# Performance work log

Measured on AMD Instinct MI355X. Metric: run time of the kernel, lower is better.

The kernel has to match this reference:

```python
import jax, jax.numpy as jnp
import numpy as np

B, NPG, C = 16, 4096, 256          # graphs, nodes per graph per type, feat dim
N = B * NPG                        # nodes per type
E = N * 16                         # edges per edge type (avg degree 16)
RATIO = 0.25
K = int(np.ceil(RATIO * NPG))      # top-k nodes per graph per type


def setup_inputs() -> dict:
    key = jax.random.key(0)
    ks = jax.random.split(key, 16)
    s = 1.0 / np.sqrt(C)
    inp = {
        "x_inst": jax.random.normal(ks[0], (N, C), jnp.float32),
        "x_data": jax.random.normal(ks[1], (N, C), jnp.float32),
        "w_kqv_inst": jax.random.normal(ks[2], (C, 3), jnp.float32) * s,
        "b_kqv_inst": jnp.zeros((3,), jnp.float32),
        "w_kqv_data": jax.random.normal(ks[3], (C, 3), jnp.float32) * s,
        "b_kqv_data": jnp.zeros((3,), jnp.float32),
        "w_out_inst": jax.random.normal(ks[4], (1, 1), jnp.float32),
        "b_out_inst": jnp.zeros((1,), jnp.float32),
        "w_out_data": jax.random.normal(ks[5], (1, 1), jnp.float32),
        "b_out_data": jnp.zeros((1,), jnp.float32),
        "krel_w": jax.random.normal(ks[6], (3,), jnp.float32),
        "krel_b": jnp.zeros((3,), jnp.float32),
        "vrel_w": jax.random.normal(ks[7], (3,), jnp.float32),
        "vrel_b": jnp.zeros((3,), jnp.float32),
        "p_rel": jnp.ones((3,), jnp.float32),
        "ei_i2d": jax.random.randint(ks[8], (2, E), 0, N, jnp.int32),
        "ei_d2i": jax.random.randint(ks[9], (2, E), 0, N, jnp.int32),
        "ei_i2i": jax.random.randint(ks[10], (2, E), 0, N, jnp.int32),
        "batch_inst": jnp.repeat(jnp.arange(B, dtype=jnp.int32), NPG),
        "batch_data": jnp.repeat(jnp.arange(B, dtype=jnp.int32), NPG),
    }
    return inp


def _hgt_scores(x_inst, x_data, w_kqv_inst, b_kqv_inst, w_kqv_data, b_kqv_data,
                w_out_inst, b_out_inst, w_out_data, b_out_data,
                krel_w, krel_b, vrel_w, vrel_b, p_rel,
                ei_i2d, ei_d2i, ei_i2i):
    # HGTConv with out_channels=1, heads=1 -> H=1, D=1 (k,q,v scalar per node)
    kqv_i = x_inst @ w_kqv_inst + b_kqv_inst   # [N,3]
    kqv_d = x_data @ w_kqv_data + b_kqv_data
    k_i, q_i, v_i = kqv_i[:, 0], kqv_i[:, 1], kqv_i[:, 2]
    k_d, q_d, v_d = kqv_d[:, 0], kqv_d[:, 1], kqv_d[:, 2]
    # dst offsets follow node-type order: inst=0, data=N
    q_glob = jnp.concatenate([q_i, q_d])       # [2N]
    Ntot = 2 * N

    def edge_terms(k_src, v_src, ei, t, dst_off):
        s, d = ei[0], ei[1]
        ke = k_src[s] * krel_w[t] + krel_b[t]  # per-relation 1x1 k_rel
        ve = v_src[s] * vrel_w[t] + vrel_b[t]  # per-relation 1x1 v_rel
        dg = d + dst_off
        logit = q_glob[dg] * ke * p_rel[t]     # (q_i*k_j).sum * p_rel / sqrt(D=1)
        return logit, ve, dg

    l0, v0, d0 = edge_terms(k_i, v_i, ei_i2d, 0, N)  # inst->data (dst=data)
    l1, v1, d1 = edge_terms(k_d, v_d, ei_d2i, 1, 0)  # data->inst (dst=inst)
    l2, v2, d2 = edge_terms(k_i, v_i, ei_i2i, 2, 0)  # inst->inst (dst=inst)
    logits = jnp.concatenate([l0, l1, l2])
    vals = jnp.concatenate([v0, v1, v2])
    dst = jnp.concatenate([d0, d1, d2])

    # segment softmax over incoming edges of each destination node
    m = jax.ops.segment_max(logits, dst, num_segments=Ntot)
    m = jnp.where(jnp.isfinite(m), m, 0.0)
    ex = jnp.exp(logits - m[dst])
    den = jax.ops.segment_sum(ex, dst, num_segments=Ntot)
    alpha = ex / den[dst]
    a = jax.ops.segment_sum(alpha * vals, dst, num_segments=Ntot)  # [2N]

    # out_lin (1->1) per node type; skip inactive (1 != 256); GELU (exact)
    s_i = jax.nn.gelu(a[:N, None] * w_out_inst[0, 0] + b_out_inst, approximate=False)
    s_d = jax.nn.gelu(a[N:, None] * w_out_data[0, 0] + b_out_data, approximate=False)
    return s_i, s_d  # [N,1] each


def _pool(x, score):
    # per-graph top-k on score, gate by tanh(score), mean over selected
    sv = score[:, 0].reshape(B, NPG)
    xv = x.reshape(B, NPG, -1)
    topv, topi = jax.lax.top_k(sv, K)                      # [B,K]
    xs = jnp.take_along_axis(xv, topi[:, :, None], axis=1)  # [B,K,C]
    return (xs * jnp.tanh(topv)[:, :, None]).mean(axis=1)   # [B,C]


def reference(x_inst, x_data, w_kqv_inst, b_kqv_inst, w_kqv_data, b_kqv_data,
              w_out_inst, b_out_inst, w_out_data, b_out_data,
              krel_w, krel_b, vrel_w, vrel_b, p_rel,
              ei_i2d, ei_d2i, ei_i2i, batch_inst, batch_data):
    # batch_* are uniform [B x NPG] blocks; pooling uses reshape equivalently.
    s_i, s_d = _hgt_scores(x_inst, x_data, w_kqv_inst, b_kqv_inst,
                           w_kqv_data, b_kqv_data, w_out_inst, b_out_inst,
                           w_out_data, b_out_data, krel_w, krel_b,
                           vrel_w, vrel_b, p_rel, ei_i2d, ei_d2i, ei_i2i)
    return jnp.concatenate([_pool(x_inst, s_i), _pool(x_data, s_d)], axis=-1)  # [B, 2C]
```

## Files before the change

### kernel.cpp

```cpp
#include <hip/hip_runtime.h>
#include <math.h>

constexpr int BB   = 16;
constexpr int NPGc = 4096;
constexpr int Cc   = 256;
constexpr int Nc   = BB * NPGc;
constexpr int Ec   = Nc * 16;
constexpr int Kc   = 1024;
constexpr int NBUK = 1024;
constexpr int BUKW = 128;
constexpr int CHUNK = 16384;
constexpr int NCHUNK = (3 * Ec) / CHUNK;

__device__ __forceinline__ unsigned long long dkey(double f) {
    long long b = __double_as_longlong(f);
    unsigned long long u = (unsigned long long)b;
    return (b < 0) ? ~u : (u | 0x8000000000000000ULL);
}
__device__ __forceinline__ double inv_dkey(unsigned long long u) {
    unsigned long long b = (u & 0x8000000000000000ULL) ? (u ^ 0x8000000000000000ULL) : ~u;
    return __longlong_as_double((long long)b);
}

__global__ __launch_bounds__(256) void kqv_kernel(
    const float* __restrict__ x_inst, const float* __restrict__ x_data,
    const float* __restrict__ w_inst, const float* __restrict__ b_inst,
    const float* __restrict__ w_data, const float* __restrict__ b_data,
    double* __restrict__ k_i, double* __restrict__ v_i,
    double* __restrict__ k_d, double* __restrict__ v_d,
    double* __restrict__ q_glob)
{
    int tid  = threadIdx.x;
    int wave = tid >> 6, lane = tid & 63;
    int grp  = lane >> 4, l = lane & 15;
    int row  = blockIdx.x * 16 + wave * 4 + grp;
    int side = (row >= Nc) ? 1 : 0;
    int node = row - side * Nc;
    const float* x  = side ? x_data : x_inst;
    const float* w  = side ? w_data : w_inst;
    const float* bb = side ? b_data : b_inst;

    const float4* rp = (const float4*)(x + (size_t)node * Cc);
    double kk = 0.0, qq = 0.0, vv = 0.0;
#pragma unroll
    for (int it = 0; it < 4; ++it) {
        float4 xv = rp[it * 16 + l];
        float xs[4] = {xv.x, xv.y, xv.z, xv.w};
        int cbase = it * 64 + l * 4;
#pragma unroll
        for (int u = 0; u < 4; ++u) {
            double xd = (double)xs[u];
            const float* wp = w + (cbase + u) * 3;
            kk += xd * (double)wp[0];
            qq += xd * (double)wp[1];
            vv += xd * (double)wp[2];
        }
    }
#pragma unroll
    for (int off = 8; off; off >>= 1) {
        kk += __shfl_xor(kk, off, 64);
        qq += __shfl_xor(qq, off, 64);
        vv += __shfl_xor(vv, off, 64);
    }
    if (l == 0) {
        kk += (double)bb[0]; qq += (double)bb[1]; vv += (double)bb[2];
        if (side) { k_d[node] = kk; v_d[node] = vv; q_glob[Nc + node] = qq; }
        else      { k_i[node] = kk; v_i[node] = vv; q_glob[node]      = qq; }
    }
}

__device__ __forceinline__ int edge_dg(const int* ei0, const int* ei1,
                                       const int* ei2, unsigned e) {
    int t = (int)(e >> 20);
    int i = (int)(e & (unsigned)(Ec - 1));
    const int* ei = (t == 0) ? ei0 : (t == 1) ? ei1 : ei2;
    int d = ei[Ec + i];
    return d + ((t == 0) ? Nc : 0);
}

__global__ __launch_bounds__(256) void count_kernel(
    const int* __restrict__ ei0, const int* __restrict__ ei1,
    const int* __restrict__ ei2, unsigned* __restrict__ bucket_cnt)
{
    __shared__ unsigned hist[NBUK];
    int tid = threadIdx.x;
    for (int j = tid; j < NBUK; j += 256) hist[j] = 0;
    __syncthreads();
    unsigned base = blockIdx.x * (unsigned)CHUNK;
#pragma unroll 4
    for (int j = 0; j < CHUNK / 256; ++j) {
        unsigned e = base + j * 256 + tid;
        int dg = edge_dg(ei0, ei1, ei2, e);
        atomicAdd(&hist[dg >> 7], 1u);
    }
    __syncthreads();
    for (int j = tid; j < NBUK; j += 256)
        if (hist[j]) atomicAdd(&bucket_cnt[j], hist[j]);
}

__global__ __launch_bounds__(1024) void scan_kernel(
    const unsigned* __restrict__ bucket_cnt,
    unsigned* __restrict__ bucket_base, unsigned* __restrict__ bucket_fill)
{
    __shared__ unsigned s[NBUK];
    int t = threadIdx.x;
    unsigned mine = bucket_cnt[t];
    s[t] = mine;
    __syncthreads();
    for (int off = 1; off < NBUK; off <<= 1) {
        unsigned v = (t >= off) ? s[t - off] : 0u;
        __syncthreads();
        s[t] += v;
        __syncthreads();
    }
    unsigned ex = s[t] - mine;
    bucket_base[t] = ex;
    bucket_fill[t] = ex;
    if (t == NBUK - 1) bucket_base[NBUK] = s[t];
}

__global__ __launch_bounds__(256) void fill_kernel(
    const int* __restrict__ ei0, const int* __restrict__ ei1,
    const int* __restrict__ ei2, unsigned* __restrict__ bucket_fill,
    unsigned* __restrict__ sorted)
{
    __shared__ unsigned hist[NBUK];
    __shared__ unsigned res[NBUK];
    int tid = threadIdx.x;
    for (int j = tid; j < NBUK; j += 256) hist[j] = 0;
    __syncthreads();
    unsigned base = blockIdx.x * (unsigned)CHUNK;
#pragma unroll 4
    for (int j = 0; j < CHUNK / 256; ++j) {
        unsigned e = base + j * 256 + tid;
        int dg = edge_dg(ei0, ei1, ei2, e);
        atomicAdd(&hist[dg >> 7], 1u);
    }
    __syncthreads();
    for (int j = tid; j < NBUK; j += 256) {
        unsigned h = hist[j];
        res[j] = h ? atomicAdd(&bucket_fill[j], h) : 0u;
        hist[j] = 0;
    }
    __syncthreads();
#pragma unroll 4
    for (int j = 0; j < CHUNK / 256; ++j) {
        unsigned e = base + j * 256 + tid;
        int t = (int)(e >> 20);
        int i = (int)(e & (unsigned)(Ec - 1));
        const int* ei = (t == 0) ? ei0 : (t == 1) ? ei1 : ei2;
        int dg = ei[Ec + i] + ((t == 0) ? Nc : 0);
        int bkt = dg >> 7;
        unsigned local = atomicAdd(&hist[bkt], 1u);
        sorted[res[bkt] + local] =
            (unsigned)i | ((unsigned)t << 20) | ((unsigned)(dg & 127) << 22);
    }
}

__global__ __launch_bounds__(256) void bucket_accum_kernel(
    const unsigned* __restrict__ bucket_base, const unsigned* __restrict__ sorted,
    const int* __restrict__ ei0, const int* __restrict__ ei1,
    const int* __restrict__ ei2,
    const float* __restrict__ krel_w, const float* __restrict__ krel_b,
    const float* __restrict__ vrel_w, const float* __restrict__ vrel_b,
    const float* __restrict__ p_rel,
    const double* __restrict__ k_i, const double* __restrict__ v_i,
    const double* __restrict__ k_d, const double* __restrict__ v_d,
    const double* __restrict__ q_glob,
    double* __restrict__ den, double* __restrict__ num)
{
    __shared__ double den_l[BUKW];
    __shared__ double num_l[BUKW];
    __shared__ double q_l[BUKW];
    int tid = threadIdx.x;
    int b   = blockIdx.x;
    if (tid < BUKW) {
        den_l[tid] = 0.0;
        num_l[tid] = 0.0;
        q_l[tid]   = q_glob[b * BUKW + tid];
    }
    double kw0 = krel_w[0], kw1 = krel_w[1], kw2 = krel_w[2];
    double kb0 = krel_b[0], kb1 = krel_b[1], kb2 = krel_b[2];
    double vw0 = vrel_w[0], vw1 = vrel_w[1], vw2 = vrel_w[2];
    double vb0 = vrel_b[0], vb1 = vrel_b[1], vb2 = vrel_b[2];
    double pr0 = p_rel[0],  pr1 = p_rel[1],  pr2 = p_rel[2];
    unsigned beg = bucket_base[b], end = bucket_base[b + 1];
    __syncthreads();

    for (unsigned e = beg + tid; e < end; e += 256) {
        unsigned r = sorted[e];
        int i    = (int)(r & 0xFFFFFu);
        int t    = (int)((r >> 20) & 3u);
        int low7 = (int)((r >> 22) & 127u);
        const int*    ei = (t == 0) ? ei0 : (t == 1) ? ei1 : ei2;
        const double* ks = (t == 1) ? k_d : k_i;
        const double* vs = (t == 1) ? v_d : v_i;
        int s = ei[i];
        double kwt = (t == 0) ? kw0 : (t == 1) ? kw1 : kw2;
        double kbt = (t == 0) ? kb0 : (t == 1) ? kb1 : kb2;
        double vwt = (t == 0) ? vw0 : (t == 1) ? vw1 : vw2;
        double vbt = (t == 0) ? vb0 : (t == 1) ? vb1 : vb2;
        double prt = (t == 0) ? pr0 : (t == 1) ? pr1 : pr2;
        double ke = ks[s] * kwt + kbt;
        double ve = vs[s] * vwt + vbt;
        double logit = q_l[low7] * ke * prt;
        double ex = exp(logit);
        atomicAdd(&den_l[low7], ex);
        atomicAdd(&num_l[low7], ex * ve);
    }
    __syncthreads();
    if (tid < BUKW) {
        den[b * BUKW + tid] = den_l[tid];
        num[b * BUKW + tid] = num_l[tid];
    }
}

__global__ __launch_bounds__(256) void select_kernel(
    const double* __restrict__ den, const double* __restrict__ num,
    const float* __restrict__ w_out_inst, const float* __restrict__ b_out_inst,
    const float* __restrict__ w_out_data, const float* __restrict__ b_out_data,
    int* __restrict__ sel_idx, float* __restrict__ sel_w)
{
    __shared__ unsigned long long keys[NPGc];
    __shared__ unsigned hist[256];
    __shared__ unsigned suf[256];
    __shared__ unsigned sh_chosen, sh_rem, sh_rem2, sh_cnt, sh_tiecnt;
    __shared__ int tie_idx[256];

    int tid  = threadIdx.x;
    int seg  = blockIdx.x;
    int side = seg >> 4;
    int b    = seg & 15;
    double wo = side ? (double)w_out_data[0] : (double)w_out_inst[0];
    double bo = side ? (double)b_out_data[0] : (double)b_out_inst[0];
    int base_node = side * Nc + b * NPGc;

    for (int ii = 0; ii < 16; ++ii) {
        int j = ii * 256 + tid;
        double dn = den[base_node + j];
        double a  = (dn > 0.0) ? num[base_node + j] / dn : 0.0;
        double z  = a * wo + bo;
        double s  = 0.5 * z * (1.0 + erf(z * 0.7071067811865476));
        keys[j] = dkey(s);
    }
    if (tid == 0) { sh_rem = Kc; sh_cnt = 0; sh_tiecnt = 0; }
    __syncthreads();

    unsigned long long prefix = 0ULL;
    for (int p = 7; p >= 0; --p) {
        hist[tid] = 0;
        __syncthreads();
        for (int ii = 0; ii < 16; ++ii) {
            unsigned long long k64 = keys[ii * 256 + tid];
            bool cand = (p == 7) || ((k64 >> ((p + 1) * 8)) == prefix);
            if (cand) atomicAdd(&hist[(unsigned)(k64 >> (p * 8)) & 255u], 1u);
        }
        __syncthreads();
        suf[tid] = hist[tid];
        __syncthreads();
        for (int ofs = 1; ofs < 256; ofs <<= 1) {
            unsigned add = (tid + ofs < 256) ? suf[tid + ofs] : 0u;
            __syncthreads();
            suf[tid] += add;
            __syncthreads();
        }
        unsigned below = (tid == 255) ? 0u : suf[tid + 1];
        if (suf[tid] >= sh_rem && below < sh_rem) {
            sh_chosen = (unsigned)tid;
            sh_rem2   = sh_rem - below;
        }
        __syncthreads();
        if (tid == 0) sh_rem = sh_rem2;
        __syncthreads();
        prefix = (prefix << 8) | (unsigned long long)sh_chosen;
    }
    unsigned long long T = prefix;
    unsigned rem = sh_rem;

    int base_sel = seg * Kc;
    for (int ii = 0; ii < 16; ++ii) {
        int j = ii * 256 + tid;
        unsigned long long k64 = keys[j];
        if (k64 > T) {
            unsigned pos = atomicAdd(&sh_cnt, 1u);
            sel_idx[base_sel + pos] = j;
            sel_w[base_sel + pos]   = (float)tanh(inv_dkey(k64));
        } else if (k64 == T) {
            unsigned tp = atomicAdd(&sh_tiecnt, 1u);
            if (tp < 256u) tie_idx[tp] = j;
        }
    }
    __syncthreads();
    unsigned tc = min(sh_tiecnt, 256u);
    float wT = (float)tanh(inv_dkey(T));
    if (tid < (int)tc) {
        int myj = tie_idx[tid];
        unsigned rank = 0;
        for (unsigned q = 0; q < tc; ++q) rank += (tie_idx[q] < myj) ? 1u : 0u;
        if (rank < rem) {
            unsigned pos = atomicAdd(&sh_cnt, 1u);
            sel_idx[base_sel + pos] = myj;
            sel_w[base_sel + pos]   = wT;
        }
    }
}

__global__ __launch_bounds__(256) void pool_kernel(
    const float* __restrict__ x_inst, const float* __restrict__ x_data,
    const int* __restrict__ sel_idx, const float* __restrict__ sel_w,
    float* __restrict__ out)
{
    __shared__ int   ridx[32];
    __shared__ float rw[32];
    int tid   = threadIdx.x;
    int seg   = blockIdx.x >> 5;
    int chunk = blockIdx.x & 31;
    int side  = seg >> 4;
    int b     = seg & 15;
    int base_sel = seg * Kc + chunk * 32;
    if (tid < 32) { ridx[tid] = sel_idx[base_sel + tid]; rw[tid] = sel_w[base_sel + tid]; }
    __syncthreads();
    const float* x = side ? x_data : x_inst;
    float acc = 0.0f;
#pragma unroll
    for (int r = 0; r < 32; ++r) {
        acc += x[((size_t)(b * NPGc + ridx[r])) * Cc + tid] * rw[r];
    }
    unsafeAtomicAdd(&out[b * 512 + side * 256 + tid], acc * (1.0f / (float)Kc));
}

extern "C" void kernel_launch(void* const* d_in, const int* in_sizes, int n_in,
                              void* d_out, int out_size, void* d_ws, size_t ws_size,
                              hipStream_t stream) {
    const float* x_inst     = (const float*)d_in[0];
    const float* x_data     = (const float*)d_in[1];
    const float* w_kqv_inst = (const float*)d_in[2];
    const float* b_kqv_inst = (const float*)d_in[3];
    const float* w_kqv_data = (const float*)d_in[4];
    const float* b_kqv_data = (const float*)d_in[5];
    const float* w_out_inst = (const float*)d_in[6];
    const float* b_out_inst = (const float*)d_in[7];
    const float* w_out_data = (const float*)d_in[8];
    const float* b_out_data = (const float*)d_in[9];
    const float* krel_w     = (const float*)d_in[10];
    const float* krel_b     = (const float*)d_in[11];
    const float* vrel_w     = (const float*)d_in[12];
    const float* vrel_b     = (const float*)d_in[13];
    const float* p_rel      = (const float*)d_in[14];
    const int*   ei_i2d     = (const int*)d_in[15];
    const int*   ei_d2i     = (const int*)d_in[16];
    const int*   ei_i2i     = (const int*)d_in[17];
    float* out = (float*)d_out;

    char* ws = (char*)d_ws;
    double* k_i    = (double*)ws;
    double* v_i    = k_i + Nc;
    double* k_d    = v_i + Nc;
    double* v_d    = k_d + Nc;
    double* q_glob = v_d + Nc;
    double* den    = q_glob + 2 * Nc;
    double* num    = den + 2 * Nc;
    unsigned* bucket_cnt  = (unsigned*)(num + 2 * Nc);
    unsigned* bucket_base = bucket_cnt + NBUK;
    unsigned* bucket_fill = bucket_base + NBUK + 1;
    int*      sel_idx     = (int*)(bucket_fill + NBUK);
    float*    sel_w       = (float*)(sel_idx + 32 * Kc);
    unsigned* sorted      = (unsigned*)(sel_w + 32 * Kc);

    hipMemsetAsync(bucket_cnt, 0, NBUK * sizeof(unsigned), stream);
    hipMemsetAsync(d_out, 0, (size_t)out_size * sizeof(float), stream);

    kqv_kernel<<<(2 * Nc) / 16, 256, 0, stream>>>(
        x_inst, x_data, w_kqv_inst, b_kqv_inst, w_kqv_data, b_kqv_data,
        k_i, v_i, k_d, v_d, q_glob);

    count_kernel<<<NCHUNK, 256, 0, stream>>>(ei_i2d, ei_d2i, ei_i2i, bucket_cnt);
    scan_kernel<<<1, NBUK, 0, stream>>>(bucket_cnt, bucket_base, bucket_fill);
    fill_kernel<<<NCHUNK, 256, 0, stream>>>(ei_i2d, ei_d2i, ei_i2i,
                                            bucket_fill, sorted);
    bucket_accum_kernel<<<NBUK, 256, 0, stream>>>(
        bucket_base, sorted, ei_i2d, ei_d2i, ei_i2i,
        krel_w, krel_b, vrel_w, vrel_b, p_rel,
        k_i, v_i, k_d, v_d, q_glob, den, num);

    select_kernel<<<32, 256, 0, stream>>>(
        den, num, w_out_inst, b_out_inst, w_out_data, b_out_data,
        sel_idx, sel_w);

    pool_kernel<<<1024, 256, 0, stream>>>(x_inst, x_data, sel_idx, sel_w, out);
}
```

Measured before the change: 360.9 us.

## Vectorize edge passes, store source ids in sorted keys, rework select and pool

The KQV kernel now has each 16-lane group process 8 rows, with the projection weights cached as doubles in registers. The count and fill kernels read destination indices as int4 and hoist the edge-type decode out of the loop. The fill kernel packs the source node id directly into the sorted entry, so the accumulation kernel no longer makes a dependent gather into the edge arrays. Top-k selection switches from eight 8-bit radix passes over 256 threads to two 11-bit passes over 1024 threads, using wave-level scans and a pairwise rank over the remaining candidates. The pool kernel uses 1024-thread blocks with float4 row loads, and the added risk is quadratic cost if many candidates share the 22-bit prefix.

```diff
diff --git a/kernel.cpp b/kernel.cpp
--- a/kernel.cpp
+++ b/kernel.cpp
@@ -33,49 +33,55 @@
     int tid  = threadIdx.x;
     int wave = tid >> 6, lane = tid & 63;
     int grp  = lane >> 4, l = lane & 15;
-    int row  = blockIdx.x * 16 + wave * 4 + grp;
-    int side = (row >= Nc) ? 1 : 0;
-    int node = row - side * Nc;
+    int g    = blockIdx.x * 16 + wave * 4 + grp;
+    int row0 = g * 8;
+    int side = (row0 >= Nc) ? 1 : 0;
+    int node0 = row0 - side * Nc;
     const float* x  = side ? x_data : x_inst;
     const float* w  = side ? w_data : w_inst;
-    const float* bb = side ? b_data : b_inst;
-
-    const float4* rp = (const float4*)(x + (size_t)node * Cc);
-    double kk = 0.0, qq = 0.0, vv = 0.0;
+    const float* bp = side ? b_data : b_inst;
+
+    double wr[48];
 #pragma unroll
     for (int it = 0; it < 4; ++it) {
-        float4 xv = rp[it * 16 + l];
-        float xs[4] = {xv.x, xv.y, xv.z, xv.w};
-        int cbase = it * 64 + l * 4;
-#pragma unroll
-        for (int u = 0; u < 4; ++u) {
-            double xd = (double)xs[u];
-            const float* wp = w + (cbase + u) * 3;
-            kk += xd * (double)wp[0];
-            qq += xd * (double)wp[1];
-            vv += xd * (double)wp[2];
-        }
-    }
-#pragma unroll
-    for (int off = 8; off; off >>= 1) {
-        kk += __shfl_xor(kk, off, 64);
-        qq += __shfl_xor(qq, off, 64);
-        vv += __shfl_xor(vv, off, 64);
-    }
-    if (l == 0) {
-        kk += (double)bb[0]; qq += (double)bb[1]; vv += (double)bb[2];
-        if (side) { k_d[node] = kk; v_d[node] = vv; q_glob[Nc + node] = qq; }
-        else      { k_i[node] = kk; v_i[node] = vv; q_glob[node]      = qq; }
-    }
-}
-
-__device__ __forceinline__ int edge_dg(const int* ei0, const int* ei1,
-                                       const int* ei2, unsigned e) {
-    int t = (int)(e >> 20);
-    int i = (int)(e & (unsigned)(Ec - 1));
-    const int* ei = (t == 0) ? ei0 : (t == 1) ? ei1 : ei2;
-    int d = ei[Ec + i];
-    return d + ((t == 0) ? Nc : 0);
+        const float4* wv = (const float4*)(w + (it * 64 + l * 4) * 3);
+        float4 f0 = wv[0], f1 = wv[1], f2 = wv[2];
+        float wt[12] = {f0.x, f0.y, f0.z, f0.w, f1.x, f1.y, f1.z, f1.w,
+                        f2.x, f2.y, f2.z, f2.w};
+#pragma unroll
+        for (int e = 0; e < 12; ++e) wr[it * 12 + e] = (double)wt[e];
+    }
+    double b0 = (double)bp[0], b1 = (double)bp[1], b2 = (double)bp[2];
+
+    const float4* rp = (const float4*)(x + (size_t)node0 * Cc);
+#pragma unroll 2
+    for (int r = 0; r < 8; ++r) {
+        double kk = 0.0, qq = 0.0, vv = 0.0;
+#pragma unroll
+        for (int it = 0; it < 4; ++it) {
+            float4 xv = rp[r * 64 + it * 16 + l];
+            float xs[4] = {xv.x, xv.y, xv.z, xv.w};
+#pragma unroll
+            for (int u = 0; u < 4; ++u) {
+                double xd = (double)xs[u];
+                kk += xd * wr[it * 12 + u * 3 + 0];
+                qq += xd * wr[it * 12 + u * 3 + 1];
+                vv += xd * wr[it * 12 + u * 3 + 2];
+            }
+        }
+#pragma unroll
+        for (int off = 8; off; off >>= 1) {
+            kk += __shfl_xor(kk, off, 64);
+            qq += __shfl_xor(qq, off, 64);
+            vv += __shfl_xor(vv, off, 64);
+        }
+        if (l == 0) {
+            int node = node0 + r;
+            kk += b0; qq += b1; vv += b2;
+            if (side) { k_d[node] = kk; v_d[node] = vv; q_glob[Nc + node] = qq; }
+            else      { k_i[node] = kk; v_i[node] = vv; q_glob[node]      = qq; }
+        }
+    }
 }
 
 __global__ __launch_bounds__(256) void count_kernel(
@@ -87,11 +93,18 @@
     for (int j = tid; j < NBUK; j += 256) hist[j] = 0;
     __syncthreads();
     unsigned base = blockIdx.x * (unsigned)CHUNK;
+    int t = (int)(base >> 20);
+    unsigned i0 = base & (unsigned)(Ec - 1);
+    const int* ei = (t == 0) ? ei0 : (t == 1) ? ei1 : ei2;
+    int off = (t == 0) ? Nc : 0;
+    const int4* dv = (const int4*)(ei + Ec + i0);
 #pragma unroll 4
-    for (int j = 0; j < CHUNK / 256; ++j) {
-        unsigned e = base + j * 256 + tid;
-        int dg = edge_dg(ei0, ei1, ei2, e);
-        atomicAdd(&hist[dg >> 7], 1u);
+    for (int j = 0; j < CHUNK / 1024; ++j) {
+        int4 d4 = dv[j * 256 + tid];
+        atomicAdd(&hist[(unsigned)(d4.x + off) >> 7], 1u);
+        atomicAdd(&hist[(unsigned)(d4.y + off) >> 7], 1u);
+        atomicAdd(&hist[(unsigned)(d4.z + off) >> 7], 1u);
+        atomicAdd(&hist[(unsigned)(d4.w + off) >> 7], 1u);
     }
     __syncthreads();
     for (int j = tid; j < NBUK; j += 256)
@@ -130,11 +143,19 @@
     for (int j = tid; j < NBUK; j += 256) hist[j] = 0;
     __syncthreads();
     unsigned base = blockIdx.x * (unsigned)CHUNK;
+    int t = (int)(base >> 20);
+    unsigned i0 = base & (unsigned)(Ec - 1);
+    const int* ei = (t == 0) ? ei0 : (t == 1) ? ei1 : ei2;
+    int off = (t == 0) ? Nc : 0;
+    const int4* dv = (const int4*)(ei + Ec + i0);
+    const int4* sv = (const int4*)(ei + i0);
 #pragma unroll 4
-    for (int j = 0; j < CHUNK / 256; ++j) {
-        unsigned e = base + j * 256 + tid;
-        int dg = edge_dg(ei0, ei1, ei2, e);
-        atomicAdd(&hist[dg >> 7], 1u);
+    for (int j = 0; j < CHUNK / 1024; ++j) {
+        int4 d4 = dv[j * 256 + tid];
+        atomicAdd(&hist[(unsigned)(d4.x + off) >> 7], 1u);
+        atomicAdd(&hist[(unsigned)(d4.y + off) >> 7], 1u);
+        atomicAdd(&hist[(unsigned)(d4.z + off) >> 7], 1u);
+        atomicAdd(&hist[(unsigned)(d4.w + off) >> 7], 1u);
     }
     __syncthreads();
     for (int j = tid; j < NBUK; j += 256) {
@@ -144,23 +165,24 @@
     }
     __syncthreads();
 #pragma unroll 4
-    for (int j = 0; j < CHUNK / 256; ++j) {
-        unsigned e = base + j * 256 + tid;
-        int t = (int)(e >> 20);
-        int i = (int)(e & (unsigned)(Ec - 1));
-        const int* ei = (t == 0) ? ei0 : (t == 1) ? ei1 : ei2;
-        int dg = ei[Ec + i] + ((t == 0) ? Nc : 0);
-        int bkt = dg >> 7;
-        unsigned local = atomicAdd(&hist[bkt], 1u);
-        sorted[res[bkt] + local] =
-            (unsigned)i | ((unsigned)t << 20) | ((unsigned)(dg & 127) << 22);
+    for (int j = 0; j < CHUNK / 1024; ++j) {
+        int4 d4 = dv[j * 256 + tid];
+        int4 s4 = sv[j * 256 + tid];
+        int dd[4] = {d4.x, d4.y, d4.z, d4.w};
+        int ss[4] = {s4.x, s4.y, s4.z, s4.w};
+#pragma unroll
+        for (int u = 0; u < 4; ++u) {
+            int dg  = dd[u] + off;
+            int bkt = dg >> 7;
+            unsigned local = atomicAdd(&hist[bkt], 1u);
+            sorted[res[bkt] + local] =
+                (unsigned)ss[u] | ((unsigned)t << 16) | ((unsigned)(dg & 127) << 18);
+        }
     }
 }
 
 __global__ __launch_bounds__(256) void bucket_accum_kernel(
     const unsigned* __restrict__ bucket_base, const unsigned* __restrict__ sorted,
-    const int* __restrict__ ei0, const int* __restrict__ ei1,
-    const int* __restrict__ ei2,
     const float* __restrict__ krel_w, const float* __restrict__ krel_b,
     const float* __restrict__ vrel_w, const float* __restrict__ vrel_b,
     const float* __restrict__ p_rel,
@@ -189,13 +211,11 @@
 
     for (unsigned e = beg + tid; e < end; e += 256) {
         unsigned r = sorted[e];
-        int i    = (int)(r & 0xFFFFFu);
-        int t    = (int)((r >> 20) & 3u);
-        int low7 = (int)((r >> 22) & 127u);
-        const int*    ei = (t == 0) ? ei0 : (t == 1) ? ei1 : ei2;
+        int s    = (int)(r & 0xFFFFu);
+        int t    = (int)((r >> 16) & 3u);
+        int low7 = (int)((r >> 18) & 127u);
         const double* ks = (t == 1) ? k_d : k_i;
         const double* vs = (t == 1) ? v_d : v_i;
-        int s = ei[i];
         double kwt = (t == 0) ? kw0 : (t == 1) ? kw1 : kw2;
         double kbt = (t == 0) ? kb0 : (t == 1) ? kb1 : kb2;
         double vwt = (t == 0) ? vw0 : (t == 1) ? vw1 : vw2;
@@ -203,10 +223,11 @@
         double prt = (t == 0) ? pr0 : (t == 1) ? pr1 : pr2;
         double ke = ks[s] * kwt + kbt;
         double ve = vs[s] * vwt + vbt;
-        double logit = q_l[low7] * ke * prt;
-        double ex = exp(logit);
-        atomicAdd(&den_l[low7], ex);
-        atomicAdd(&num_l[low7], ex * ve);
+        double ex = exp(q_l[low7] * ke * prt);
+        __hip_atomic_fetch_add(&den_l[low7], ex, __ATOMIC_RELAXED,
+                               __HIP_MEMORY_SCOPE_WORKGROUP);
+        __hip_atomic_fetch_add(&num_l[low7], ex * ve, __ATOMIC_RELAXED,
+                               __HIP_MEMORY_SCOPE_WORKGROUP);
     }
     __syncthreads();
     if (tid < BUKW) {
@@ -215,17 +236,17 @@
     }
 }
 
-__global__ __launch_bounds__(256) void select_kernel(
+__global__ __launch_bounds__(1024) void select_kernel(
     const double* __restrict__ den, const double* __restrict__ num,
     const float* __restrict__ w_out_inst, const float* __restrict__ b_out_inst,
     const float* __restrict__ w_out_data, const float* __restrict__ b_out_data,
     int* __restrict__ sel_idx, float* __restrict__ sel_w)
 {
     __shared__ unsigned long long keys[NPGc];
-    __shared__ unsigned hist[256];
-    __shared__ unsigned suf[256];
-    __shared__ unsigned sh_chosen, sh_rem, sh_rem2, sh_cnt, sh_tiecnt;
-    __shared__ int tie_idx[256];
+    __shared__ unsigned hist[2048];
+    __shared__ unsigned wsum[16];
+    __shared__ unsigned short cand[NPGc];
+    __shared__ unsigned sh_bin1, sh_rem1, sh_bin2, sh_rem2, sh_cnt, sh_nc;
 
     int tid  = threadIdx.x;
     int seg  = blockIdx.x;
@@ -234,99 +255,167 @@
     double wo = side ? (double)w_out_data[0] : (double)w_out_inst[0];
     double bo = side ? (double)b_out_data[0] : (double)b_out_inst[0];
     int base_node = side * Nc + b * NPGc;
-
-    for (int ii = 0; ii < 16; ++ii) {
-        int j = ii * 256 + tid;
+    int base_sel  = seg * Kc;
+
+    unsigned long long myk[4]; int myj[4];
+#pragma unroll
+    for (int p = 0; p < 4; ++p) {
+        int j = p * 1024 + tid;
         double dn = den[base_node + j];
         double a  = (dn > 0.0) ? num[base_node + j] / dn : 0.0;
         double z  = a * wo + bo;
         double s  = 0.5 * z * (1.0 + erf(z * 0.7071067811865476));
-        keys[j] = dkey(s);
-    }
-    if (tid == 0) { sh_rem = Kc; sh_cnt = 0; sh_tiecnt = 0; }
-    __syncthreads();
-
-    unsigned long long prefix = 0ULL;
-    for (int p = 7; p >= 0; --p) {
-        hist[tid] = 0;
-        __syncthreads();
-        for (int ii = 0; ii < 16; ++ii) {
-            unsigned long long k64 = keys[ii * 256 + tid];
-            bool cand = (p == 7) || ((k64 >> ((p + 1) * 8)) == prefix);
-            if (cand) atomicAdd(&hist[(unsigned)(k64 >> (p * 8)) & 255u], 1u);
-        }
-        __syncthreads();
-        suf[tid] = hist[tid];
-        __syncthreads();
-        for (int ofs = 1; ofs < 256; ofs <<= 1) {
-            unsigned add = (tid + ofs < 256) ? suf[tid + ofs] : 0u;
-            __syncthreads();
-            suf[tid] += add;
-            __syncthreads();
-        }
-        unsigned below = (tid == 255) ? 0u : suf[tid + 1];
-        if (suf[tid] >= sh_rem && below < sh_rem) {
-            sh_chosen = (unsigned)tid;
-            sh_rem2   = sh_rem - below;
-        }
-        __syncthreads();
-        if (tid == 0) sh_rem = sh_rem2;
-        __syncthreads();
-        prefix = (prefix << 8) | (unsigned long long)sh_chosen;
-    }
-    unsigned long long T = prefix;
-    unsigned rem = sh_rem;
-
-    int base_sel = seg * Kc;
-    for (int ii = 0; ii < 16; ++ii) {
-        int j = ii * 256 + tid;
+        unsigned long long k64 = dkey(s);
+        keys[j] = k64; myk[p] = k64; myj[p] = j;
+    }
+    if (tid == 0) { sh_cnt = 0; sh_nc = 0; }
+    hist[tid] = 0; hist[tid + 1024] = 0;
+    __syncthreads();
+
+#pragma unroll
+    for (int p = 0; p < 4; ++p) atomicAdd(&hist[(unsigned)(myk[p] >> 53)], 1u);
+    __syncthreads();
+    {
+        unsigned g0 = hist[2047 - 2 * tid];
+        unsigned g1 = hist[2046 - 2 * tid];
+        unsigned x = g0 + g1;
+        int lane = tid & 63;
+#pragma unroll
+        for (int off = 1; off < 64; off <<= 1) {
+            unsigned y = __shfl_up(x, off, 64);
+            if (lane >= off) x += y;
+        }
+        if (lane == 63) wsum[tid >> 6] = x;
+        __syncthreads();
+        if (tid < 16) {
+            unsigned v = wsum[tid];
+#pragma unroll
+            for (int off = 1; off < 16; off <<= 1) {
+                unsigned y = __shfl_up(v, off, 64);
+                if (tid >= off) v += y;
+            }
+            wsum[tid] = v;
+        }
+        __syncthreads();
+        unsigned basew = (tid >= 64) ? wsum[(tid >> 6) - 1] : 0u;
+        unsigned incl  = basew + x;
+        unsigned incl0 = incl - g1;
+        unsigned K = Kc;
+        if (incl0 >= K && incl0 - g0 < K) { sh_bin1 = 2047 - 2 * tid; sh_rem1 = K - (incl0 - g0); }
+        if (incl  >= K && incl  - g1 < K) { sh_bin1 = 2046 - 2 * tid; sh_rem1 = K - (incl  - g1); }
+    }
+    __syncthreads();
+    unsigned bin1 = sh_bin1, rem1 = sh_rem1;
+    hist[tid] = 0; hist[tid + 1024] = 0;
+    __syncthreads();
+
+#pragma unroll
+    for (int p = 0; p < 4; ++p)
+        if ((unsigned)(myk[p] >> 53) == bin1)
+            atomicAdd(&hist[(unsigned)(myk[p] >> 42) & 2047u], 1u);
+    __syncthreads();
+    {
+        unsigned g0 = hist[2047 - 2 * tid];
+        unsigned g1 = hist[2046 - 2 * tid];
+        unsigned x = g0 + g1;
+        int lane = tid & 63;
+#pragma unroll
+        for (int off = 1; off < 64; off <<= 1) {
+            unsigned y = __shfl_up(x, off, 64);
+            if (lane >= off) x += y;
+        }
+        if (lane == 63) wsum[tid >> 6] = x;
+        __syncthreads();
+        if (tid < 16) {
+            unsigned v = wsum[tid];
+#pragma unroll
+            for (int off = 1; off < 16; off <<= 1) {
+                unsigned y = __shfl_up(v, off, 64);
+                if (tid >= off) v += y;
+            }
+            wsum[tid] = v;
+        }
+        __syncthreads();
+        unsigned basew = (tid >= 64) ? wsum[(tid >> 6) - 1] : 0u;
+        unsigned incl  = basew + x;
+        unsigned incl0 = incl - g1;
+        unsigned K = rem1;
+        if (incl0 >= K && incl0 - g0 < K) { sh_bin2 = 2047 - 2 * tid; sh_rem2 = K - (incl0 - g0); }
+        if (incl  >= K && incl  - g1 < K) { sh_bin2 = 2046 - 2 * tid; sh_rem2 = K - (incl  - g1); }
+    }
+    __syncthreads();
+    unsigned long long pref22 = ((unsigned long long)bin1 << 11) | (unsigned long long)sh_bin2;
+    unsigned rem2 = sh_rem2;
+
+#pragma unroll
+    for (int p = 0; p < 4; ++p) {
+        unsigned long long top22 = myk[p] >> 42;
+        if (top22 > pref22) {
+            unsigned pos = atomicAdd(&sh_cnt, 1u);
+            sel_idx[base_sel + pos] = myj[p];
+            sel_w[base_sel + pos]   = (float)tanh(inv_dkey(myk[p]));
+        } else if (top22 == pref22) {
+            unsigned cp = atomicAdd(&sh_nc, 1u);
+            cand[cp] = (unsigned short)myj[p];
+        }
+    }
+    __syncthreads();
+
+    unsigned nc = sh_nc;
+    for (unsigned c = tid; c < nc; c += 1024) {
+        int j = cand[c];
         unsigned long long k64 = keys[j];
-        if (k64 > T) {
+        unsigned rank = 0;
+        for (unsigned q = 0; q < nc; ++q) {
+            int jq = cand[q];
+            unsigned long long kq = keys[jq];
+            rank += (kq > k64 || (kq == k64 && jq < j)) ? 1u : 0u;
+        }
+        if (rank < rem2) {
             unsigned pos = atomicAdd(&sh_cnt, 1u);
             sel_idx[base_sel + pos] = j;
             sel_w[base_sel + pos]   = (float)tanh(inv_dkey(k64));
-        } else if (k64 == T) {
-            unsigned tp = atomicAdd(&sh_tiecnt, 1u);
-            if (tp < 256u) tie_idx[tp] = j;
-        }
-    }
-    __syncthreads();
-    unsigned tc = min(sh_tiecnt, 256u);
-    float wT = (float)tanh(inv_dkey(T));
-    if (tid < (int)tc) {
-        int myj = tie_idx[tid];
-        unsigned rank = 0;
-        for (unsigned q = 0; q < tc; ++q) rank += (tie_idx[q] < myj) ? 1u : 0u;
-        if (rank < rem) {
-            unsigned pos = atomicAdd(&sh_cnt, 1u);
-            sel_idx[base_sel + pos] = myj;
-            sel_w[base_sel + pos]   = wT;
-        }
-    }
-}
-
-__global__ __launch_bounds__(256) void pool_kernel(
+        }
+    }
+}
+
+__global__ __launch_bounds__(1024) void pool_kernel(
     const float* __restrict__ x_inst, const float* __restrict__ x_data,
     const int* __restrict__ sel_idx, const float* __restrict__ sel_w,
     float* __restrict__ out)
 {
-    __shared__ int   ridx[32];
-    __shared__ float rw[32];
+    __shared__ int   ridx[128];
+    __shared__ float rw[128];
+    __shared__ float accs[256];
     int tid   = threadIdx.x;
-    int seg   = blockIdx.x >> 5;
-    int chunk = blockIdx.x & 31;
+    int blk   = blockIdx.x;
+    int seg   = blk >> 3;
+    int chunk = blk & 7;
     int side  = seg >> 4;
     int b     = seg & 15;
-    int base_sel = seg * Kc + chunk * 32;
-    if (tid < 32) { ridx[tid] = sel_idx[base_sel + tid]; rw[tid] = sel_w[base_sel + tid]; }
+    if (tid < 128) {
+        ridx[tid] = sel_idx[seg * Kc + chunk * 128 + tid];
+        rw[tid]   = sel_w[seg * Kc + chunk * 128 + tid];
+    }
+    if (tid < 256) accs[tid] = 0.0f;
     __syncthreads();
     const float* x = side ? x_data : x_inst;
-    float acc = 0.0f;
-#pragma unroll
-    for (int r = 0; r < 32; ++r) {
-        acc += x[((size_t)(b * NPGc + ridx[r])) * Cc + tid] * rw[r];
-    }
-    unsafeAtomicAdd(&out[b * 512 + side * 256 + tid], acc * (1.0f / (float)Kc));
+    int w = tid >> 6, l = tid & 63;
+    float ax = 0.f, ay = 0.f, az = 0.f, aw = 0.f;
+#pragma unroll
+    for (int r = 0; r < 8; ++r) {
+        int   row = ridx[w * 8 + r];
+        float wt  = rw[w * 8 + r];
+        float4 xv = ((const float4*)(x + ((size_t)(b * NPGc + row)) * Cc))[l];
+        ax += xv.x * wt; ay += xv.y * wt; az += xv.z * wt; aw += xv.w * wt;
+    }
+    atomicAdd(&accs[l * 4 + 0], ax);
+    atomicAdd(&accs[l * 4 + 1], ay);
+    atomicAdd(&accs[l * 4 + 2], az);
+    atomicAdd(&accs[l * 4 + 3], aw);
+    __syncthreads();
+    if (tid < 256)
+        unsafeAtomicAdd(&out[b * 512 + side * 256 + tid], accs[tid] * (1.0f / (float)Kc));
 }
 
 extern "C" void kernel_launch(void* const* d_in, const int* in_sizes, int n_in,
@@ -370,22 +459,23 @@
     hipMemsetAsync(bucket_cnt, 0, NBUK * sizeof(unsigned), stream);
     hipMemsetAsync(d_out, 0, (size_t)out_size * sizeof(float), stream);
 
-    kqv_kernel<<<(2 * Nc) / 16, 256, 0, stream>>>(
-        x_inst, x_data, w_kqv_inst, b_kqv_inst, w_kqv_data, b_kqv_data,
-        k_i, v_i, k_d, v_d, q_glob);
-
     count_kernel<<<NCHUNK, 256, 0, stream>>>(ei_i2d, ei_d2i, ei_i2i, bucket_cnt);
     scan_kernel<<<1, NBUK, 0, stream>>>(bucket_cnt, bucket_base, bucket_fill);
     fill_kernel<<<NCHUNK, 256, 0, stream>>>(ei_i2d, ei_d2i, ei_i2i,
                                             bucket_fill, sorted);
+
+    kqv_kernel<<<(2 * Nc) / 128, 256, 0, stream>>>(
+        x_inst, x_data, w_kqv_inst, b_kqv_inst, w_kqv_data, b_kqv_data,
+        k_i, v_i, k_d, v_d, q_glob);
+
     bucket_accum_kernel<<<NBUK, 256, 0, stream>>>(
-        bucket_base, sorted, ei_i2d, ei_d2i, ei_i2i,
+        bucket_base, sorted,
         krel_w, krel_b, vrel_w, vrel_b, p_rel,
         k_i, v_i, k_d, v_d, q_glob, den, num);
 
-    select_kernel<<<32, 256, 0, stream>>>(
+    select_kernel<<<32, 1024, 0, stream>>>(
         den, num, w_out_inst, b_out_inst, w_out_data, b_out_data,
         sel_idx, sel_w);
 
-    pool_kernel<<<1024, 256, 0, stream>>>(x_inst, x_data, sel_idx, sel_w, out);
-}
+    pool_kernel<<<256, 1024, 0, stream>>>(x_inst, x_data, sel_idx, sel_w, out);
+}
```

New measurement: 323.0 us. 1.12x faster.
